# Kernel optimization log

Measured on AMD Instinct MI355X. Metric: run time of the kernel, lower is better.

Reference implementation:

```python
import jax, jax.numpy as jnp
import numpy as np

HID = 64; H = 2; D = 32; L = 2; G = 64; F_IN = 771
NA = 120000; NE = 60000; E0 = 1500000; E1 = 1000000; E2 = 1000000


def _seg_mean(x, seg, n):
    s = jax.ops.segment_sum(x, seg, num_segments=n)
    c = jax.ops.segment_sum(jnp.ones((x.shape[0], 1), x.dtype), seg, num_segments=n)
    return s / jnp.maximum(c, 1.0)


def setup_inputs() -> dict:
    ks = jax.random.split(jax.random.key(0), 32)
    r = lambda i, s: 0.02 * jax.random.normal(ks[i], s, jnp.float32)
    z = lambda s: jnp.zeros(s, jnp.float32)
    inp = {}
    inp['x_argument'] = jax.random.normal(ks[0], (NA, F_IN), jnp.float32)
    inp['x_evidence'] = jax.random.normal(ks[1], (NE, F_IN), jnp.float32)
    inp['Win'] = r(2, (2, F_IN, HID)); inp['b_in'] = z((2, HID))
    inp['Wk'] = r(3, (L, 2, HID, HID)); inp['bk'] = z((L, 2, HID))
    inp['Wq'] = r(4, (L, 2, HID, HID)); inp['bq'] = z((L, 2, HID))
    inp['Wv'] = r(5, (L, 2, HID, HID)); inp['bv'] = z((L, 2, HID))
    inp['Wa'] = r(6, (L, 2, HID, HID)); inp['ba'] = z((L, 2, HID))
    inp['skip'] = jnp.ones((L, 2), jnp.float32)
    inp['Watt'] = r(7, (L, 3, H, D, D)); inp['Wmsg'] = r(8, (L, 3, H, D, D))
    inp['prel'] = jnp.ones((L, 3, H), jnp.float32)
    inp['Wnews'] = r(9, (384, HID)); inp['bnews'] = z((HID,))
    inp['Wdeb'] = r(10, (HID, HID)); inp['bdeb'] = z((HID,))
    inp['Wqm'] = r(11, (HID, HID)); inp['bqm'] = z((HID,))
    inp['Wkm'] = r(12, (HID, HID)); inp['bkm'] = z((HID,))
    inp['Wvm'] = r(13, (HID, HID)); inp['bvm'] = z((HID,))
    inp['Wom'] = r(14, (HID, HID)); inp['bom'] = z((HID,))
    inp['Wc1'] = r(15, (2 * HID, 64)); inp['bc1'] = z((64,))
    inp['Wc2'] = r(16, (64, 1)); inp['bc2'] = z((1,))
    inp['e0_src'] = jax.random.randint(ks[17], (E0,), 0, NA)
    inp['e0_dst'] = jax.random.randint(ks[18], (E0,), 0, NA)
    inp['e1_src'] = jax.random.randint(ks[19], (E1,), 0, NE)
    inp['e1_dst'] = jax.random.randint(ks[20], (E1,), 0, NA)
    inp['e2_src'] = jax.random.randint(ks[21], (E2,), 0, NA)
    inp['e2_dst'] = jax.random.randint(ks[22], (E2,), 0, NE)
    inp['batch_arg'] = jnp.sort(jax.random.randint(ks[23], (NA,), 0, G))
    return inp


def reference(x_argument, x_evidence, Win, b_in, Wk, bk, Wq, bq, Wv, bv, Wa, ba,
              skip, Watt, Wmsg, prel, Wnews, bnews, Wdeb, bdeb,
              Wqm, bqm, Wkm, bkm, Wvm, bvm, Wom, bom, Wc1, bc1, Wc2, bc2,
              e0_src, e0_dst, e1_src, e1_dst, e2_src, e2_dst, batch_arg):
    # Claim embedding from RAW features (slice 384:768), pooled per graph.
    claim_raw = _seg_mean(x_argument[:, 384:768], batch_arg, G)
    # Per-node-type input projection + ReLU. type 0 = argument, 1 = evidence.
    xs = [jax.nn.relu(x_argument @ Win[0] + b_in[0]),
          jax.nn.relu(x_evidence @ Win[1] + b_in[1])]
    # (src_type, dst_type, src_idx, dst_idx) for each heterogeneous edge type.
    edges = [(0, 0, e0_src, e0_dst), (1, 0, e1_src, e1_dst), (0, 1, e2_src, e2_dst)]
    scale = 1.0 / jnp.sqrt(jnp.float32(D))
    for l in range(L):  # HGTConv stack
        Kt = [(xs[t] @ Wk[l, t] + bk[l, t]).reshape(-1, H, D) for t in range(2)]
        Qt = [(xs[t] @ Wq[l, t] + bq[l, t]).reshape(-1, H, D) for t in range(2)]
        Vt = [(xs[t] @ Wv[l, t] + bv[l, t]).reshape(-1, H, D) for t in range(2)]
        buf = {0: [], 1: []}
        for e, (s, d, src, dst) in enumerate(edges):
            k2 = jnp.einsum('ehd,hdf->ehf', Kt[s][src], Watt[l, e])  # relation key transform
            v2 = jnp.einsum('ehd,hdf->ehf', Vt[s][src], Wmsg[l, e])  # relation msg transform
            sc = (Qt[d][dst] * k2).sum(-1) * prel[l, e] * scale      # (E, H)
            buf[d].append((sc, dst, v2))
        new_xs = []
        for d in range(2):
            n = xs[d].shape[0]
            sc = jnp.concatenate([b[0] for b in buf[d]], 0)
            dst = jnp.concatenate([b[1] for b in buf[d]], 0)
            v2 = jnp.concatenate([b[2] for b in buf[d]], 0)
            # segment softmax over all incoming edges of each destination node
            m = jax.ops.segment_max(sc, dst, num_segments=n)
            ex = jnp.exp(sc - m[dst])
            den = jax.ops.segment_sum(ex, dst, num_segments=n)
            alpha = ex / den[dst]
            agg = jax.ops.segment_sum(alpha[..., None] * v2, dst, num_segments=n).reshape(n, HID)
            out = jax.nn.gelu(agg, approximate=False) @ Wa[l, d] + ba[l, d]
            beta = jax.nn.sigmoid(skip[l, d])
            new_xs.append(beta * out + (1.0 - beta) * xs[d])
        xs = new_xs
    graph_emb = _seg_mean(xs[0], batch_arg, G)
    eF = claim_raw @ Wnews + bnews          # (G, HID)
    g = graph_emb @ Wdeb + bdeb             # (G, HID)
    # MultiheadAttention with query len 1 and key len 1: softmax over a single
    # key is identically 1, so attn_out == out_proj(v_proj(g)) exactly
    # (Wqm/bqm/Wkm/bkm receive exactly zero gradient, matching torch).
    v = g @ Wvm + bvm
    attn_out = v @ Wom + bom
    h = jax.nn.relu(jnp.concatenate([g, attn_out], -1) @ Wc1 + bc1)  # dropout is eval-mode identity
    return h @ Wc2 + bc2  # (G, 1)
```

## Files before the change

kernel.cpp:

```cpp
#include <hip/hip_runtime.h>
#include <math.h>

#define N0 120000
#define N1 60000
#define E0N 1500000
#define E1N 1000000
#define E2N 1000000
#define FIN 771
#define NG 64
#define KSTEPS_IN 25

#define GB0 ((N0 + 127) / 128)
#define GB1 ((N1 + 127) / 128)
#define AB0 ((N0 + 3) / 4)
#define AB1 ((N1 + 3) / 4)
#define SB0 ((N0 + 1023) / 1024)
#define SB1 ((N1 + 1023) / 1024)

#define Q0O   ((size_t)0)
#define KV00O ((size_t)N0 * 64)
#define KV02O ((size_t)N0 * 192)
#define Q1O   ((size_t)N0 * 320)
#define KV11O ((size_t)N0 * 320 + (size_t)N1 * 64)

typedef __attribute__((ext_vector_type(8))) short short8;
typedef __attribute__((ext_vector_type(4))) float f32x4;
typedef __attribute__((ext_vector_type(4))) unsigned short ushort4v;
typedef unsigned short ushort;

__device__ __forceinline__ float gelu_f(float v) {
    return 0.5f * v * (1.f + erff(v * 0.70710678118654752f));
}
__device__ __forceinline__ ushort f2b(float f) {
    union { float f; unsigned u; } v; v.f = f;
    unsigned u = v.u;
    return (ushort)((u + 0x7FFFu + ((u >> 16) & 1u)) >> 16);
}
__device__ __forceinline__ float lo16(unsigned u) {
    union { unsigned x; float f; } v; v.x = u << 16; return v.f;
}
__device__ __forceinline__ float hi16(unsigned u) {
    union { unsigned x; float f; } v; v.x = u & 0xFFFF0000u; return v.f;
}
__device__ __forceinline__ int asi(float f) { union { float f; int i; } v; v.f = f; return v.i; }
__device__ __forceinline__ float asf(int i) { union { int i; float f; } v; v.i = i; return v.f; }

__global__ __launch_bounds__(256) void in_proj_all(
    const float* __restrict__ xa, const float* __restrict__ xe,
    const ushort* __restrict__ Wpin, const float* __restrict__ b_in,
    float* __restrict__ xs0, float* __restrict__ xs1)
{
    __shared__ ushort xt[2][128 * 40];
    const int bx = blockIdx.x;
    const int type = (bx >= GB0) ? 1 : 0;
    const float* __restrict__ x = type ? xe : xa;
    const int nrows = type ? N1 : N0;
    const ushort* __restrict__ Wp = Wpin + (type ? (size_t)KSTEPS_IN * 2048 : 0);
    const float* __restrict__ bias = b_in + type * 64;
    float* __restrict__ out = type ? xs1 : xs0;
    const int r0 = (type ? bx - GB0 : bx) * 128;

    const int tid = threadIdx.x;
    const int w = tid >> 6, lane = tid & 63;
    const int lrow = w * 32;
    const int srow = tid >> 4;
    const int kp = (tid & 15) * 2;
    f32x4 acc[2][4] = {};

    auto stage = [&](int ks, int buf) {
        const int k0 = ks * 32;
        #pragma unroll
        for (int p = 0; p < 8; ++p) {
            int row = srow + p * 16;
            int gr = r0 + row;
            float a0 = 0.f, a1 = 0.f;
            if (gr < nrows) {
                int k = k0 + kp;
                const float* xr = x + (size_t)gr * FIN;
                if (k < FIN) a0 = xr[k];
                if (k + 1 < FIN) a1 = xr[k + 1];
            }
            *(unsigned*)&xt[buf][row * 40 + kp] = (unsigned)f2b(a0) | ((unsigned)f2b(a1) << 16);
        }
    };

    stage(0, 0);
    __syncthreads();
    for (int ks = 0; ks < KSTEPS_IN; ++ks) {
        if (ks + 1 < KSTEPS_IN) stage(ks + 1, (ks + 1) & 1);
        const ushort* xb = xt[ks & 1];
        short8 bfr[2];
        #pragma unroll
        for (int rb = 0; rb < 2; ++rb)
            bfr[rb] = *(const short8*)&xb[(lrow + rb * 16 + (lane & 15)) * 40 + (lane >> 4) * 8];
        const ushort* wb = Wp + (size_t)ks * 2048 + lane * 8;
        #pragma unroll
        for (int cg = 0; cg < 4; ++cg) {
            short8 afr = *(const short8*)&wb[cg * 512];
            acc[0][cg] = __builtin_amdgcn_mfma_f32_16x16x32_bf16(afr, bfr[0], acc[0][cg], 0, 0, 0);
            acc[1][cg] = __builtin_amdgcn_mfma_f32_16x16x32_bf16(afr, bfr[1], acc[1][cg], 0, 0, 0);
        }
        __syncthreads();
    }
    const int c0b = (lane >> 4) * 4;
    #pragma unroll
    for (int rb = 0; rb < 2; ++rb) {
        int r = r0 + lrow + rb * 16 + (lane & 15);
        if (r < nrows) {
            #pragma unroll
            for (int cg = 0; cg < 4; ++cg) {
                int c = cg * 16 + c0b;
                float4 o;
                o.x = fmaxf(acc[rb][cg][0] + bias[c + 0], 0.f);
                o.y = fmaxf(acc[rb][cg][1] + bias[c + 1], 0.f);
                o.z = fmaxf(acc[rb][cg][2] + bias[c + 2], 0.f);
                o.w = fmaxf(acc[rb][cg][3] + bias[c + 3], 0.f);
                *(float4*)&out[(size_t)r * 64 + c] = o;
            }
        }
    }
}

__global__ __launch_bounds__(256) void proj_fused(
    const float* __restrict__ xs0, const float* __restrict__ xs1,
    const ushort* __restrict__ Wpack, const float* __restrict__ bpack,
    ushort* __restrict__ projAll, int l)
{
    const int bx = blockIdx.x;
    const int type = (bx >= GB0) ? 1 : 0;
    const float* __restrict__ in = type ? xs1 : xs0;
    const int nrows = type ? N1 : N0;
    const int tid = threadIdx.x, w = tid >> 6, lane = tid & 63;
    const int r0 = (type ? bx - GB0 : bx) * 128 + w * 32;

    short8 bfr[2][2];
    #pragma unroll
    for (int ksp = 0; ksp < 2; ++ksp) {
        #pragma unroll
        for (int rb = 0; rb < 2; ++rb) {
            int gr = min(r0 + rb * 16 + (lane & 15), nrows - 1);
            const float* src = in + (size_t)gr * 64 + ksp * 32 + (lane >> 4) * 8;
            float4 f0 = *(const float4*)src;
            float4 f1 = *(const float4*)(src + 4);
            short8 t;
            t[0] = (short)f2b(f0.x); t[1] = (short)f2b(f0.y);
            t[2] = (short)f2b(f0.z); t[3] = (short)f2b(f0.w);
            t[4] = (short)f2b(f1.x); t[5] = (short)f2b(f1.y);
            t[6] = (short)f2b(f1.z); t[7] = (short)f2b(f1.w);
            bfr[ksp][rb] = t;
        }
    }

    const int nslots = type ? 3 : 5;
    const int sbase = l * 8 + (type ? 5 : 0);
    const int c0b = (lane >> 4) * 4;

    for (int slot = 0; slot < nslots; ++slot) {
        const ushort* Wp = Wpack + (size_t)(sbase + slot) * 4096;
        const float* bias = bpack + (size_t)(sbase + slot) * 64;
        size_t ooff; unsigned pitch, qs, ph;
        if (slot == 0) { ooff = type ? Q1O : Q0O; pitch = 64; qs = 4; ph = 0; }
        else {
            int kv = (slot + 1) >> 1;
            ooff = type ? KV11O : (kv == 1 ? KV00O : KV02O);
            pitch = 128; qs = 8; ph = (slot & 1) ? 0u : 4u;
        }
        ushort* out = projAll + ooff;
        f32x4 acc[2][4] = {};
        #pragma unroll
        for (int ksp = 0; ksp < 2; ++ksp) {
            const ushort* wb = Wp + ksp * 2048 + lane * 8;
            #pragma unroll
            for (int cg = 0; cg < 4; ++cg) {
                short8 afr = *(const short8*)&wb[cg * 512];
                acc[0][cg] = __builtin_amdgcn_mfma_f32_16x16x32_bf16(afr, bfr[ksp][0], acc[0][cg], 0, 0, 0);
                acc[1][cg] = __builtin_amdgcn_mfma_f32_16x16x32_bf16(afr, bfr[ksp][1], acc[1][cg], 0, 0, 0);
            }
        }
        #pragma unroll
        for (int rb = 0; rb < 2; ++rb) {
            int r = r0 + rb * 16 + (lane & 15);
            if (r < nrows) {
                #pragma unroll
                for (int cg = 0; cg < 4; ++cg) {
                    int c = cg * 16 + c0b;
                    ushort4v o;
                    o[0] = f2b(acc[rb][cg][0] + bias[c + 0]);
                    o[1] = f2b(acc[rb][cg][1] + bias[c + 1]);
                    o[2] = f2b(acc[rb][cg][2] + bias[c + 2]);
                    o[3] = f2b(acc[rb][cg][3] + bias[c + 3]);
                    *(ushort4v*)&out[(size_t)r * pitch + (unsigned)(c >> 2) * qs + ph] = o;
                }
            }
        }
    }
}

__global__ __launch_bounds__(256) void epi_fused(
    const float* __restrict__ agg0, const float* __restrict__ agg1,
    const ushort* __restrict__ WaPack, const float* __restrict__ ba,
    float* __restrict__ xs0, float* __restrict__ xs1,
    const float* __restrict__ skip, int l)
{
    const int bx = blockIdx.x;
    const int type = (bx >= GB0) ? 1 : 0;
    const float* __restrict__ in = type ? agg1 : agg0;
    float* __restrict__ xs = type ? xs1 : xs0;
    const int nrows = type ? N1 : N0;
    const ushort* __restrict__ Wp = WaPack + (size_t)(l * 2 + type) * 4096;
    const float* __restrict__ bias = ba + (size_t)(l * 2 + type) * 64;
    const float beta = 1.f / (1.f + __expf(-skip[l * 2 + type]));

    const int tid = threadIdx.x, w = tid >> 6, lane = tid & 63;
    const int r0 = (type ? bx - GB0 : bx) * 128 + w * 32;
    f32x4 acc[2][4] = {};
    #pragma unroll
    for (int ksp = 0; ksp < 2; ++ksp) {
        short8 bfr[2];
        #pragma unroll
        for (int rb = 0; rb < 2; ++rb) {
            int gr = min(r0 + rb * 16 + (lane & 15), nrows - 1);
            const float* src = in + (size_t)gr * 64 + ksp * 32 + (lane >> 4) * 8;
            float4 f0 = *(const float4*)src;
            float4 f1 = *(const float4*)(src + 4);
            short8 t;
            t[0] = (short)f2b(gelu_f(f0.x)); t[1] = (short)f2b(gelu_f(f0.y));
            t[2] = (short)f2b(gelu_f(f0.z)); t[3] = (short)f2b(gelu_f(f0.w));
            t[4] = (short)f2b(gelu_f(f1.x)); t[5] = (short)f2b(gelu_f(f1.y));
            t[6] = (short)f2b(gelu_f(f1.z)); t[7] = (short)f2b(gelu_f(f1.w));
            bfr[rb] = t;
        }
        const ushort* wb = Wp + ksp * 2048 + lane * 8;
        #pragma unroll
        for (int cg = 0; cg < 4; ++cg) {
            short8 afr = *(const short8*)&wb[cg * 512];
            acc[0][cg] = __builtin_amdgcn_mfma_f32_16x16x32_bf16(afr, bfr[0], acc[0][cg], 0, 0, 0);
            acc[1][cg] = __builtin_amdgcn_mfma_f32_16x16x32_bf16(afr, bfr[1], acc[1][cg], 0, 0, 0);
        }
    }
    const int c0b = (lane >> 4) * 4;
    #pragma unroll
    for (int rb = 0; rb < 2; ++rb) {
        int r = r0 + rb * 16 + (lane & 15);
        if (r < nrows) {
            #pragma unroll
            for (int cg = 0; cg < 4; ++cg) {
                int c = cg * 16 + c0b;
                float4 xo = *(const float4*)&xs[(size_t)r * 64 + c];
                float4 o;
                o.x = beta * (acc[rb][cg][0] + bias[c + 0]) + (1.f - beta) * xo.x;
                o.y = beta * (acc[rb][cg][1] + bias[c + 1]) + (1.f - beta) * xo.y;
                o.z = beta * (acc[rb][cg][2] + bias[c + 2]) + (1.f - beta) * xo.z;
                o.w = beta * (acc[rb][cg][3] + bias[c + 3]) + (1.f - beta) * xo.w;
                *(float4*)&xs[(size_t)r * 64 + c] = o;
            }
        }
    }
}

__global__ __launch_bounds__(256) void prep_kernel(
    const float* __restrict__ Wq, const float* __restrict__ bq,
    const float* __restrict__ Wk, const float* __restrict__ bk,
    const float* __restrict__ Wv, const float* __restrict__ bv,
    const float* __restrict__ Watt, const float* __restrict__ Wmsg,
    const float* __restrict__ prel, const float* __restrict__ Win,
    const float* __restrict__ Wa,
    ushort* __restrict__ Wpack, float* __restrict__ bpack,
    ushort* __restrict__ Wpin, ushort* __restrict__ WaPack)
{
    __shared__ float WF[4096];
    const int b = blockIdx.x;
    const int tid = threadIdx.x;
    if (b < 16) {
        const int l = b >> 3;
        const int slot = b & 7;
        const float SCALE = 0.17677669529663689f;
        ushort* outW = Wpack + (size_t)(l * 8 + slot) * 4096;
        float* outB = bpack + (size_t)(l * 8 + slot) * 64;
        const float *Wsrc = 0, *bsrc = 0, *A = 0, *prelE = 0;
        int copy = 0;
        switch (slot) {
            case 0: Wsrc = Wq + (l*2+0)*4096; bsrc = bq + (l*2+0)*64; copy = 1; break;
            case 5: Wsrc = Wq + (l*2+1)*4096; bsrc = bq + (l*2+1)*64; copy = 1; break;
            case 1: Wsrc = Wk + (l*2+0)*4096; bsrc = bk + (l*2+0)*64; A = Watt + (l*3+0)*2048; prelE = prel + l*6 + 0; break;
            case 2: Wsrc = Wv + (l*2+0)*4096; bsrc = bv + (l*2+0)*64; A = Wmsg + (l*3+0)*2048; break;
            case 3: Wsrc = Wk + (l*2+0)*4096; bsrc = bk + (l*2+0)*64; A = Watt + (l*3+2)*2048; prelE = prel + l*6 + 4; break;
            case 4: Wsrc = Wv + (l*2+0)*4096; bsrc = bv + (l*2+0)*64; A = Wmsg + (l*3+2)*2048; break;
            case 6: Wsrc = Wk + (l*2+1)*4096; bsrc = bk + (l*2+1)*64; A = Watt + (l*3+1)*2048; prelE = prel + l*6 + 2; break;
            case 7: Wsrc = Wv + (l*2+1)*4096; bsrc = bv + (l*2+1)*64; A = Wmsg + (l*3+1)*2048; break;
        }
        if (copy) {
            for (int idx = tid; idx < 4096; idx += 256) WF[idx] = Wsrc[idx];
            if (tid < 64) outB[tid] = bsrc[tid];
        } else {
            for (int idx = tid; idx < 4096; idx += 256) {
                int k = idx >> 6, c = idx & 63, h = c >> 5, f = c & 31;
                float s = 0.f;
                for (int d = 0; d < 32; ++d)
                    s += Wsrc[k * 64 + h * 32 + d] * A[(h * 32 + d) * 32 + f];
                if (prelE) s *= prelE[h] * SCALE;
                WF[idx] = s;
            }
            if (tid < 64) {
                int h = tid >> 5, f = tid & 31;
                float s = 0.f;
                for (int d = 0; d < 32; ++d)
                    s += bsrc[h * 32 + d] * A[(h * 32 + d) * 32 + f];
                if (prelE) s *= prelE[h] * SCALE;
                outB[tid] = s;
            }
        }
        __syncthreads();
        for (int idx = tid; idx < 4096; idx += 256) {
            int ksp = idx >> 11, rem = idx & 2047;
            int cg = rem >> 9, rem2 = rem & 511;
            int lane = rem2 >> 3, j = rem2 & 7;
            int k = ksp * 32 + (lane >> 4) * 8 + j;
            int c = cg * 16 + (lane & 15);
            outW[idx] = f2b(WF[k * 64 + c]);
        }
    } else if (b < 16 + 2 * KSTEPS_IN) {
        const int pb = b - 16;
        const int type = pb / KSTEPS_IN, ks = pb % KSTEPS_IN;
        const float* W = Win + (size_t)type * FIN * 64;
        ushort* out = Wpin + (size_t)pb * 2048;
        for (int idx = tid; idx < 2048; idx += 256) {
            int cg = idx >> 9, rem = idx & 511, lane = rem >> 3, j = rem & 7;
            int k = ks * 32 + (lane >> 4) * 8 + j;
            int c = cg * 16 + (lane & 15);
            out[idx] = f2b((k < FIN) ? W[(size_t)k * 64 + c] : 0.f);
        }
    } else {
        const int mb = b - 16 - 2 * KSTEPS_IN;
        const float* W = Wa + (size_t)mb * 4096;
        ushort* o = WaPack + (size_t)mb * 4096;
        for (int idx = tid; idx < 4096; idx += 256) {
            int ksp = idx >> 11, rem = idx & 2047;
            int cg = rem >> 9, rem2 = rem & 511;
            int lane = rem2 >> 3, j = rem2 & 7;
            int k = ksp * 32 + (lane >> 4) * 8 + j;
            int c = cg * 16 + (lane & 15);
            o[idx] = f2b(W[k * 64 + c]);
        }
    }
}

__global__ void zero4_kernel(int* __restrict__ c0, int* __restrict__ c1,
                             int* __restrict__ gs, int* __restrict__ gc)
{
    int i = blockIdx.x * blockDim.x + threadIdx.x;
    if (i < N0) c0[i] = 0;
    else if (i < N0 + N1) c1[i - N0] = 0;
    else if (i < N0 + N1 + NG * 64) gs[i - N0 - N1] = 0;
    else if (i < N0 + N1 + NG * 64 + NG) gc[i - N0 - N1 - NG * 64] = 0;
}
__global__ void zero2_kernel(int* __restrict__ c0, int* __restrict__ c1)
{
    int i = blockIdx.x * blockDim.x + threadIdx.x;
    if (i < N0) c0[i] = 0;
    else if (i < N0 + N1) c1[i - N0] = 0;
}

__global__ void hist_all_kernel(
    const int* __restrict__ e0d, const int* __restrict__ e1d, const int* __restrict__ e2d,
    int* __restrict__ cnt0, int* __restrict__ cnt1)
{
    const int total = E0N + E1N + E2N;
    for (int i = blockIdx.x * blockDim.x + threadIdx.x; i < total; i += gridDim.x * blockDim.x) {
        if (i < E0N) atomicAdd(&cnt0[e0d[i]], 1);
        else if (i < E0N + E1N) atomicAdd(&cnt0[e1d[i - E0N]], 1);
        else atomicAdd(&cnt1[e2d[i - E0N - E1N]], 1);
    }
}

__global__ __launch_bounds__(256) void scan1_all_kernel(
    const int* __restrict__ cnt0, const int* __restrict__ cnt1,
    int* __restrict__ off0, int* __restrict__ off1,
    int* __restrict__ bsA, int* __restrict__ bsB)
{
    __shared__ int sa[256], sb[256];
    const int tid = threadIdx.x;
    const int b = blockIdx.x;
    const int* cnt; int n; int* off; int* bsum; int lb;
    if (b < SB0) { cnt = cnt0; n = N0; off = off0; bsum = bsA; lb = b; }
    else { cnt = cnt1; n = N1; off = off1; bsum = bsB; lb = b - SB0; }
    const int base = lb * 1024 + tid * 4;
    int v[4];
    int run = 0;
    #pragma unroll
    for (int i = 0; i < 4; ++i) {
        int x = (base + i < n) ? cnt[base + i] : 0;
        run += x; v[i] = run;
    }
    sa[tid] = run;
    __syncthreads();
    int* src = sa; int* dst = sb;
    for (int d = 1; d < 256; d <<= 1) {
        int x = src[tid];
        if (tid >= d) x += src[tid - d];
        dst[tid] = x;
        __syncthreads();
        int* t = src; src = dst; dst = t;
    }
    int excl = src[tid] - run;
    #pragma unroll
    for (int i = 0; i < 4; ++i)
        if (base + i < n) off[base + i + 1] = excl + v[i];
    if (tid == 255) bsum[lb] = src[255];
}

__global__ __launch_bounds__(256) void scan2_all_kernel(int* __restrict__ bsA, int* __restrict__ bsB)
{
    __shared__ int sa[256], sb[256];
    const int tid = threadIdx.x;
    int* bsum = blockIdx.x ? bsB : bsA;
    const int nb = blockIdx.x ? SB1 : SB0;
    int x = (tid < nb) ? bsum[tid] : 0;
    sa[tid] = x;
    __syncthreads();
    int* src = sa; int* dst = sb;
    for (int d = 1; d < 256; d <<= 1) {
        int y = src[tid];
        if (tid >= d) y += src[tid - d];
        dst[tid] = y;
        __syncthreads();
        int* t = src; src = dst; dst = t;
    }
    if (tid < nb) bsum[tid] = src[tid] - x;
}

__global__ __launch_bounds__(256) void scan3_all_kernel(
    int* __restrict__ off0, int* __restrict__ off1,
    const int* __restrict__ bsA, const int* __restrict__ bsB)
{
    const int b = blockIdx.x;
    int* off; const int* boff; int n; int lb;
    if (b < SB0) { off = off0; boff = bsA; n = N0; lb = b; }
    else { off = off1; boff = bsB; n = N1; lb = b - SB0; }
    const int base = lb * 1024 + threadIdx.x * 4;
    const int add = boff[lb];
    #pragma unroll
    for (int i = 0; i < 4; ++i)
        if (base + i < n) off[base + i + 1] += add;
    if (lb == 0 && threadIdx.x == 0) off[0] = 0;
}

__global__ void scatter_all_kernel(
    const int* __restrict__ e0s, const int* __restrict__ e0d,
    const int* __restrict__ e1s, const int* __restrict__ e1d,
    const int* __restrict__ e2s, const int* __restrict__ e2d,
    const int* __restrict__ off0, const int* __restrict__ off1,
    int* __restrict__ cnt0, int* __restrict__ cnt1,
    int* __restrict__ rec0, int* __restrict__ rec1)
{
    const int total = E0N + E1N + E2N;
    for (int i = blockIdx.x * blockDim.x + threadIdx.x; i < total; i += gridDim.x * blockDim.x) {
        if (i < E0N) {
            int d = e0d[i];
            int pos = off0[d] + atomicAdd(&cnt0[d], 1);
            rec0[pos] = e0s[i];
        } else if (i < E0N + E1N) {
            int k = i - E0N;
            int d = e1d[k];
            int pos = off0[d] + atomicAdd(&cnt0[d], 1);
            rec0[pos] = e1s[k] | (1 << 20);
        } else {
            int k = i - E0N - E1N;
            int d = e2d[k];
            int pos = off1[d] + atomicAdd(&cnt1[d], 1);
            rec1[pos] = e2s[k];
        }
    }
}

__global__ __launch_bounds__(256) void agg_fused(
    const int* __restrict__ off0, const int* __restrict__ rec0,
    const int* __restrict__ off1, const int* __restrict__ rec1,
    const ushort* __restrict__ projAll,
    float* __restrict__ agg0, float* __restrict__ agg1)
{
    const int bx = blockIdx.x;
    const int type = (bx >= AB0) ? 1 : 0;
    const int lane = threadIdx.x & 63;
    const int node = (type ? bx - AB0 : bx) * 4 + (threadIdx.x >> 6);
    const int ndst = type ? N1 : N0;
    if (node >= ndst) return;
    const int* __restrict__ off = type ? off1 : off0;
    const int* __restrict__ rec = type ? rec1 : rec0;
    const ushort* __restrict__ Q   = projAll + (type ? Q1O : Q0O);
    const ushort* __restrict__ KVa = projAll + (type ? KV02O : KV00O);
    const ushort* __restrict__ KVb = projAll + (type ? KV02O : KV11O);
    float* __restrict__ outAgg = type ? agg1 : agg0;

    const int grp = lane >> 4;
    const int gi  = lane & 15;
    float q0, q1, q2, q3;
    {
        const unsigned* qp = (const unsigned*)(Q + (size_t)node * 64 + gi * 4);
        unsigned u0 = qp[0], u1 = qp[1];
        q0 = lo16(u0); q1 = hi16(u0); q2 = lo16(u1); q3 = hi16(u1);
    }
    const int s = off[node], e = off[node + 1];
    float den = 0.f, a0 = 0.f, a1 = 0.f, a2 = 0.f, a3 = 0.f;
    for (int j = s; j < e; j += 8) {
        int jj0 = j + grp, jj1 = jj0 + 4;
        bool v0 = jj0 < e, v1 = jj1 < e;
        int r0 = rec[v0 ? jj0 : s];
        int r1 = rec[v1 ? jj1 : s];
        const ushort* KV0 = (r0 & (1 << 20)) ? KVb : KVa;
        const ushort* KV1 = (r1 & (1 << 20)) ? KVb : KVa;
        uint4 kv0 = *(const uint4*)(KV0 + ((size_t)(unsigned)(r0 & 0xFFFFF) << 7) + gi * 8);
        uint4 kv1 = *(const uint4*)(KV1 + ((size_t)(unsigned)(r1 & 0xFFFFF) << 7) + gi * 8);
        float p0 = lo16(kv0.x) * q0 + hi16(kv0.x) * q1 + lo16(kv0.y) * q2 + hi16(kv0.y) * q3;
        float p1 = lo16(kv1.x) * q0 + hi16(kv1.x) * q1 + lo16(kv1.y) * q2 + hi16(kv1.y) * q3;
        p0 += asf(__builtin_amdgcn_ds_swizzle(asi(p0), 0x041F));
        p1 += asf(__builtin_amdgcn_ds_swizzle(asi(p1), 0x041F));
        p0 += asf(__builtin_amdgcn_ds_swizzle(asi(p0), 0x081F));
        p1 += asf(__builtin_amdgcn_ds_swizzle(asi(p1), 0x081F));
        p0 += asf(__builtin_amdgcn_ds_swizzle(asi(p0), 0x101F));
        p1 += asf(__builtin_amdgcn_ds_swizzle(asi(p1), 0x101F));
        float w0 = v0 ? __expf(p0) : 0.f;
        float w1 = v1 ? __expf(p1) : 0.f;
        den += w0 + w1;
        a0 = fmaf(w0, lo16(kv0.z), a0); a0 = fmaf(w1, lo16(kv1.z), a0);
        a1 = fmaf(w0, hi16(kv0.z), a1); a1 = fmaf(w1, hi16(kv1.z), a1);
        a2 = fmaf(w0, lo16(kv0.w), a2); a2 = fmaf(w1, lo16(kv1.w), a2);
        a3 = fmaf(w0, hi16(kv0.w), a3); a3 = fmaf(w1, hi16(kv1.w), a3);
    }
    a0 += __shfl_xor(a0, 16); a0 += __shfl_xor(a0, 32);
    a1 += __shfl_xor(a1, 16); a1 += __shfl_xor(a1, 32);
    a2 += __shfl_xor(a2, 16); a2 += __shfl_xor(a2, 32);
    a3 += __shfl_xor(a3, 16); a3 += __shfl_xor(a3, 32);
    den += __shfl_xor(den, 16); den += __shfl_xor(den, 32);
    if (lane < 16) {
        float inv = (den > 0.f) ? 1.f / den : 0.f;
        float4 o;
        o.x = a0 * inv; o.y = a1 * inv; o.z = a2 * inv; o.w = a3 * inv;
        *(float4*)&outAgg[(size_t)node * 64 + gi * 4] = o;
    }
}

__global__ __launch_bounds__(256) void segsum_kernel(
    const float* __restrict__ xs, const int* __restrict__ seg, int n,
    float* __restrict__ gsum, int* __restrict__ gcnt)
{
    const int lane = threadIdx.x & 63;
    const int wid = blockIdx.x * 4 + (threadIdx.x >> 6);
    const int rbeg = wid * 256;
    if (rbeg >= n) return;
    const int rend = min(rbeg + 256, n);
    float s = 0.f;
    int cur = seg[rbeg];
    int run = 0;
    for (int r = rbeg; r < rend; ++r) {
        int sg = seg[r];
        if (sg != cur) {
            atomicAdd(&gsum[cur * 64 + lane], s);
            if (lane == 0) atomicAdd(&gcnt[cur], run);
            cur = sg; s = 0.f; run = 0;
        }
        s += xs[(size_t)r * 64 + lane];
        run++;
    }
    atomicAdd(&gsum[cur * 64 + lane], s);
    if (lane == 0) atomicAdd(&gcnt[cur], run);
}

__global__ __launch_bounds__(256) void head_kernel(
    const float* __restrict__ gsum, const int* __restrict__ gcnt,
    const float* __restrict__ Wdeb, const float* __restrict__ bdeb,
    const float* __restrict__ Wvm, const float* __restrict__ bvm,
    const float* __restrict__ Wom, const float* __restrict__ bom,
    const float* __restrict__ Wc1, const float* __restrict__ bc1,
    const float* __restrict__ Wc2, const float* __restrict__ bc2,
    float* __restrict__ outp)
{
    __shared__ float A[4096], B[4096], C[4096];
    const int tid = threadIdx.x;
    for (int idx = tid; idx < 4096; idx += 256) {
        int g = idx >> 6;
        A[idx] = gsum[idx] / fmaxf((float)gcnt[g], 1.f);
    }
    __syncthreads();
    for (int idx = tid; idx < 4096; idx += 256) {
        int g = idx >> 6, c = idx & 63;
        float s = bdeb[c];
        for (int k = 0; k < 64; ++k) s = fmaf(A[g * 64 + k], Wdeb[k * 64 + c], s);
        B[idx] = s;
    }
    __syncthreads();
    for (int idx = tid; idx < 4096; idx += 256) {
        int g = idx >> 6, c = idx & 63;
        float s = bvm[c];
        for (int k = 0; k < 64; ++k) s = fmaf(B[g * 64 + k], Wvm[k * 64 + c], s);
        C[idx] = s;
    }
    __syncthreads();
    for (int idx = tid; idx < 4096; idx += 256) {
        int g = idx >> 6, c = idx & 63;
        float s = bom[c];
        for (int k = 0; k < 64; ++k) s = fmaf(C[g * 64 + k], Wom[k * 64 + c], s);
        A[idx] = s;
    }
    __syncthreads();
    for (int idx = tid; idx < 4096; idx += 256) {
        int g = idx >> 6, c = idx & 63;
        float s = bc1[c];
        for (int k = 0; k < 64; ++k) s = fmaf(B[g * 64 + k], Wc1[k * 64 + c], s);
        for (int k = 0; k < 64; ++k) s = fmaf(A[g * 64 + k], Wc1[(64 + k) * 64 + c], s);
        C[idx] = fmaxf(s, 0.f);
    }
    __syncthreads();
    if (tid < 64) {
        float s = bc2[0];
        for (int c = 0; c < 64; ++c) s = fmaf(C[tid * 64 + c], Wc2[c], s);
        outp[tid] = s;
    }
}

extern "C" void kernel_launch(void* const* d_in, const int* in_sizes, int n_in,
                              void* d_out, int out_size, void* d_ws, size_t ws_size,
                              hipStream_t stream)
{
    const float* x_arg = (const float*)d_in[0];
    const float* x_ev  = (const float*)d_in[1];
    const float* Win   = (const float*)d_in[2];
    const float* b_in  = (const float*)d_in[3];
    const float* Wk    = (const float*)d_in[4];
    const float* bk    = (const float*)d_in[5];
    const float* Wq    = (const float*)d_in[6];
    const float* bq    = (const float*)d_in[7];
    const float* Wv    = (const float*)d_in[8];
    const float* bv    = (const float*)d_in[9];
    const float* Wa    = (const float*)d_in[10];
    const float* ba    = (const float*)d_in[11];
    const float* skip  = (const float*)d_in[12];
    const float* Watt  = (const float*)d_in[13];
    const float* Wmsg  = (const float*)d_in[14];
    const float* prel  = (const float*)d_in[15];
    const float* Wdeb  = (const float*)d_in[18];
    const float* bdeb  = (const float*)d_in[19];
    const float* Wvm   = (const float*)d_in[24];
    const float* bvm   = (const float*)d_in[25];
    const float* Wom   = (const float*)d_in[26];
    const float* bom   = (const float*)d_in[27];
    const float* Wc1   = (const float*)d_in[28];
    const float* bc1   = (const float*)d_in[29];
    const float* Wc2   = (const float*)d_in[30];
    const float* bc2   = (const float*)d_in[31];
    const int* e0s = (const int*)d_in[32];
    const int* e0d = (const int*)d_in[33];
    const int* e1s = (const int*)d_in[34];
    const int* e1d = (const int*)d_in[35];
    const int* e2s = (const int*)d_in[36];
    const int* e2d = (const int*)d_in[37];
    const int* batch = (const int*)d_in[38];
    float* outp = (float*)d_out;

    char* w = (char*)d_ws;
    size_t o = 0;
    auto alloc = [&](size_t bytes) -> char* {
        char* p = w + o;
        o = (o + bytes + 255) & ~(size_t)255;
        return p;
    };
    float* xs0   = (float*)alloc((size_t)N0 * 64 * 4);
    float* xs1   = (float*)alloc((size_t)N1 * 64 * 4);
    ushort* projAll = (ushort*)alloc(((size_t)N0 * 320 + (size_t)N1 * 192) * 2);
    float* agg0  = (float*)alloc((size_t)N0 * 64 * 4);
    float* agg1  = (float*)alloc((size_t)N1 * 64 * 4);
    int* off0 = (int*)alloc((size_t)(N0 + 1) * 4);
    int* off1 = (int*)alloc((size_t)(N1 + 1) * 4);
    int* cnt0 = (int*)alloc((size_t)N0 * 4);
    int* cnt1 = (int*)alloc((size_t)N1 * 4);
    int* rec0 = (int*)alloc((size_t)(E0N + E1N) * 4);
    int* rec1 = (int*)alloc((size_t)E2N * 4);
    int* bsA  = (int*)alloc(256 * 4);
    int* bsB  = (int*)alloc(256 * 4);
    ushort* Wpack = (ushort*)alloc((size_t)16 * 4096 * 2);
    float* bpack = (float*)alloc((size_t)16 * 64 * 4);
    ushort* Wpin = (ushort*)alloc((size_t)2 * KSTEPS_IN * 2048 * 2);
    ushort* WaPack = (ushort*)alloc((size_t)4 * 4096 * 2);
    float* gsum = (float*)alloc((size_t)NG * 64 * 4);
    int* gcnt = (int*)alloc((size_t)NG * 4);
    if (o > ws_size) return;

    prep_kernel<<<16 + 2 * KSTEPS_IN + 4, 256, 0, stream>>>(
        Wq, bq, Wk, bk, Wv, bv, Watt, Wmsg, prel, Win, Wa, Wpack, bpack, Wpin, WaPack);
    zero4_kernel<<<(N0 + N1 + NG * 64 + NG + 255) / 256, 256, 0, stream>>>(
        cnt0, cnt1, (int*)gsum, gcnt);
    hist_all_kernel<<<2048, 256, 0, stream>>>(e0d, e1d, e2d, cnt0, cnt1);
    scan1_all_kernel<<<SB0 + SB1, 256, 0, stream>>>(cnt0, cnt1, off0, off1, bsA, bsB);
    scan2_all_kernel<<<2, 256, 0, stream>>>(bsA, bsB);
    scan3_all_kernel<<<SB0 + SB1, 256, 0, stream>>>(off0, off1, bsA, bsB);
    zero2_kernel<<<(N0 + N1 + 255) / 256, 256, 0, stream>>>(cnt0, cnt1);
    scatter_all_kernel<<<2048, 256, 0, stream>>>(
        e0s, e0d, e1s, e1d, e2s, e2d, off0, off1, cnt0, cnt1, rec0, rec1);
    in_proj_all<<<GB0 + GB1, 256, 0, stream>>>(x_arg, x_ev, Wpin, b_in, xs0, xs1);
    for (int l = 0; l < 2; ++l) {
        proj_fused<<<GB0 + GB1, 256, 0, stream>>>(xs0, xs1, Wpack, bpack, projAll, l);
        agg_fused<<<AB0 + AB1, 256, 0, stream>>>(off0, rec0, off1, rec1, projAll, agg0, agg1);
        epi_fused<<<GB0 + GB1, 256, 0, stream>>>(agg0, agg1, WaPack, ba, xs0, xs1, skip, l);
    }
    {
        int waves = (N0 + 255) / 256;
        segsum_kernel<<<(waves + 3) / 4, 256, 0, stream>>>(xs0, batch, N0, gsum, gcnt);
    }
    head_kernel<<<1, 256, 0, stream>>>(gsum, gcnt, Wdeb, bdeb, Wvm, bvm, Wom, bom,
                                       Wc1, bc1, Wc2, bc2, outp);
}
```

Before: 1.174 ms.

## Load input features straight into MFMA fragments and fold count reset into scan

The input projection no longer stages rows through double-buffered shared memory with block barriers. Each lane now loads its own 8 consecutive floats per k-step directly from global memory into registers, prefetching one step ahead, and converts them to bf16 MFMA operands. The 3-element tail is handled separately. The loads become unaligned vector reads, and the access pattern within a wave is less coalesced across rows. Separately, the histogram counts are reset inside the first scan kernel, which removes one kernel launch.

```diff
diff --git a/kernel.cpp b/kernel.cpp
--- a/kernel.cpp
+++ b/kernel.cpp
@@ -25,6 +25,7 @@
 
 typedef __attribute__((ext_vector_type(8))) short short8;
 typedef __attribute__((ext_vector_type(4))) float f32x4;
+typedef float f32x4u __attribute__((ext_vector_type(4), aligned(4)));
 typedef __attribute__((ext_vector_type(4))) unsigned short ushort4v;
 typedef unsigned short ushort;
 
@@ -50,7 +51,6 @@
     const ushort* __restrict__ Wpin, const float* __restrict__ b_in,
     float* __restrict__ xs0, float* __restrict__ xs1)
 {
-    __shared__ ushort xt[2][128 * 40];
     const int bx = blockIdx.x;
     const int type = (bx >= GB0) ? 1 : 0;
     const float* __restrict__ x = type ? xe : xa;
@@ -58,54 +58,66 @@
     const ushort* __restrict__ Wp = Wpin + (type ? (size_t)KSTEPS_IN * 2048 : 0);
     const float* __restrict__ bias = b_in + type * 64;
     float* __restrict__ out = type ? xs1 : xs0;
-    const int r0 = (type ? bx - GB0 : bx) * 128;
-
-    const int tid = threadIdx.x;
-    const int w = tid >> 6, lane = tid & 63;
-    const int lrow = w * 32;
-    const int srow = tid >> 4;
-    const int kp = (tid & 15) * 2;
+
+    const int tid = threadIdx.x, w = tid >> 6, lane = tid & 63;
+    const int r0 = (type ? bx - GB0 : bx) * 128 + w * 32;
+
+    const int rA = min(r0 + (lane & 15), nrows - 1);
+    const int rB = min(r0 + 16 + (lane & 15), nrows - 1);
+    const float* __restrict__ xA = x + (size_t)rA * FIN + (lane >> 4) * 8;
+    const float* __restrict__ xB = x + (size_t)rB * FIN + (lane >> 4) * 8;
+
     f32x4 acc[2][4] = {};
-
-    auto stage = [&](int ks, int buf) {
-        const int k0 = ks * 32;
+    f32x4u cA0 = *(const f32x4u*)xA;
+    f32x4u cA1 = *(const f32x4u*)(xA + 4);
+    f32x4u cB0 = *(const f32x4u*)xB;
+    f32x4u cB1 = *(const f32x4u*)(xB + 4);
+
+    for (int ks = 0; ks < 24; ++ks) {
+        f32x4u nA0 = {}, nA1 = {}, nB0 = {}, nB1 = {};
+        if (ks < 23) {
+            const float* pA = xA + (ks + 1) * 32;
+            const float* pB = xB + (ks + 1) * 32;
+            nA0 = *(const f32x4u*)pA; nA1 = *(const f32x4u*)(pA + 4);
+            nB0 = *(const f32x4u*)pB; nB1 = *(const f32x4u*)(pB + 4);
+        }
+        short8 bA, bB;
         #pragma unroll
-        for (int p = 0; p < 8; ++p) {
-            int row = srow + p * 16;
-            int gr = r0 + row;
-            float a0 = 0.f, a1 = 0.f;
-            if (gr < nrows) {
-                int k = k0 + kp;
-                const float* xr = x + (size_t)gr * FIN;
-                if (k < FIN) a0 = xr[k];
-                if (k + 1 < FIN) a1 = xr[k + 1];
-            }
-            *(unsigned*)&xt[buf][row * 40 + kp] = (unsigned)f2b(a0) | ((unsigned)f2b(a1) << 16);
-        }
-    };
-
-    stage(0, 0);
-    __syncthreads();
-    for (int ks = 0; ks < KSTEPS_IN; ++ks) {
-        if (ks + 1 < KSTEPS_IN) stage(ks + 1, (ks + 1) & 1);
-        const ushort* xb = xt[ks & 1];
-        short8 bfr[2];
-        #pragma unroll
-        for (int rb = 0; rb < 2; ++rb)
-            bfr[rb] = *(const short8*)&xb[(lrow + rb * 16 + (lane & 15)) * 40 + (lane >> 4) * 8];
+        for (int j = 0; j < 4; ++j) {
+            bA[j]     = (short)f2b(cA0[j]);
+            bA[j + 4] = (short)f2b(cA1[j]);
+            bB[j]     = (short)f2b(cB0[j]);
+            bB[j + 4] = (short)f2b(cB1[j]);
+        }
         const ushort* wb = Wp + (size_t)ks * 2048 + lane * 8;
         #pragma unroll
         for (int cg = 0; cg < 4; ++cg) {
             short8 afr = *(const short8*)&wb[cg * 512];
-            acc[0][cg] = __builtin_amdgcn_mfma_f32_16x16x32_bf16(afr, bfr[0], acc[0][cg], 0, 0, 0);
-            acc[1][cg] = __builtin_amdgcn_mfma_f32_16x16x32_bf16(afr, bfr[1], acc[1][cg], 0, 0, 0);
-        }
-        __syncthreads();
+            acc[0][cg] = __builtin_amdgcn_mfma_f32_16x16x32_bf16(afr, bA, acc[0][cg], 0, 0, 0);
+            acc[1][cg] = __builtin_amdgcn_mfma_f32_16x16x32_bf16(afr, bB, acc[1][cg], 0, 0, 0);
+        }
+        cA0 = nA0; cA1 = nA1; cB0 = nB0; cB1 = nB1;
+    }
+    {
+        short8 bA = {}, bB = {};
+        if ((lane >> 4) == 0) {
+            const float* tA = x + (size_t)rA * FIN + 768;
+            const float* tB = x + (size_t)rB * FIN + 768;
+            bA[0] = (short)f2b(tA[0]); bA[1] = (short)f2b(tA[1]); bA[2] = (short)f2b(tA[2]);
+            bB[0] = (short)f2b(tB[0]); bB[1] = (short)f2b(tB[1]); bB[2] = (short)f2b(tB[2]);
+        }
+        const ushort* wb = Wp + (size_t)24 * 2048 + lane * 8;
+        #pragma unroll
+        for (int cg = 0; cg < 4; ++cg) {
+            short8 afr = *(const short8*)&wb[cg * 512];
+            acc[0][cg] = __builtin_amdgcn_mfma_f32_16x16x32_bf16(afr, bA, acc[0][cg], 0, 0, 0);
+            acc[1][cg] = __builtin_amdgcn_mfma_f32_16x16x32_bf16(afr, bB, acc[1][cg], 0, 0, 0);
+        }
     }
     const int c0b = (lane >> 4) * 4;
     #pragma unroll
     for (int rb = 0; rb < 2; ++rb) {
-        int r = r0 + lrow + rb * 16 + (lane & 15);
+        int r = r0 + rb * 16 + (lane & 15);
         if (r < nrows) {
             #pragma unroll
             for (int cg = 0; cg < 4; ++cg) {
@@ -354,12 +366,6 @@
     else if (i < N0 + N1 + NG * 64) gs[i - N0 - N1] = 0;
     else if (i < N0 + N1 + NG * 64 + NG) gc[i - N0 - N1 - NG * 64] = 0;
 }
-__global__ void zero2_kernel(int* __restrict__ c0, int* __restrict__ c1)
-{
-    int i = blockIdx.x * blockDim.x + threadIdx.x;
-    if (i < N0) c0[i] = 0;
-    else if (i < N0 + N1) c1[i - N0] = 0;
-}
 
 __global__ void hist_all_kernel(
     const int* __restrict__ e0d, const int* __restrict__ e1d, const int* __restrict__ e2d,
@@ -374,14 +380,14 @@
 }
 
 __global__ __launch_bounds__(256) void scan1_all_kernel(
-    const int* __restrict__ cnt0, const int* __restrict__ cnt1,
+    int* __restrict__ cnt0, int* __restrict__ cnt1,
     int* __restrict__ off0, int* __restrict__ off1,
     int* __restrict__ bsA, int* __restrict__ bsB)
 {
     __shared__ int sa[256], sb[256];
     const int tid = threadIdx.x;
     const int b = blockIdx.x;
-    const int* cnt; int n; int* off; int* bsum; int lb;
+    int* cnt; int n; int* off; int* bsum; int lb;
     if (b < SB0) { cnt = cnt0; n = N0; off = off0; bsum = bsA; lb = b; }
     else { cnt = cnt1; n = N1; off = off1; bsum = bsB; lb = b - SB0; }
     const int base = lb * 1024 + tid * 4;
@@ -392,6 +398,9 @@
         int x = (base + i < n) ? cnt[base + i] : 0;
         run += x; v[i] = run;
     }
+    #pragma unroll
+    for (int i = 0; i < 4; ++i)
+        if (base + i < n) cnt[base + i] = 0;
     sa[tid] = run;
     __syncthreads();
     int* src = sa; int* dst = sb;
@@ -693,7 +702,6 @@
     scan1_all_kernel<<<SB0 + SB1, 256, 0, stream>>>(cnt0, cnt1, off0, off1, bsA, bsB);
     scan2_all_kernel<<<2, 256, 0, stream>>>(bsA, bsB);
     scan3_all_kernel<<<SB0 + SB1, 256, 0, stream>>>(off0, off1, bsA, bsB);
-    zero2_kernel<<<(N0 + N1 + 255) / 256, 256, 0, stream>>>(cnt0, cnt1);
     scatter_all_kernel<<<2048, 256, 0, stream>>>(
         e0s, e0d, e1s, e1d, e2s, e2d, off0, off1, cnt0, cnt1, rec0, rec1);
     in_proj_all<<<GB0 + GB1, 256, 0, stream>>>(x_arg, x_ev, Wpin, b_in, xs0, xs1);
```

Result: faster. 1.063 ms (-9.4%).
